# Kernel optimization log

Hardware: AMD Instinct MI355X
Metric: run time of the kernel (lower is better)

Reference implementation:

```python
import jax, jax.numpy as jnp
import numpy as np

NUM_FEATURES = 128   # conv spatial length
WINDOW = 128         # conv channels / lstm seq len
KC = 16              # kernels per group
KS = 3               # conv kernel size
FC1 = 32             # number of independent LSTMs
H = 32               # lstm hidden size
NL = 2               # lstm layers
PAD = 1
POOL_LEN = (NUM_FEATURES + 2 * PAD) // 2  # maxpool(k=2,s=2,p=1) output length
B = 128


def setup_inputs():
    key = jax.random.key(0)
    ks = jax.random.split(key, 13)
    x = jax.random.normal(ks[0], (B, WINDOW, NUM_FEATURES), jnp.float32)
    conv_w = jax.random.normal(ks[1], (WINDOW * KC, 1, KS), jnp.float32) * 0.3
    conv_b = jax.random.normal(ks[2], (WINDOW * KC,), jnp.float32) * 0.1
    fc1_in = KC * POOL_LEN
    fc1_w = jax.random.normal(ks[3], (FC1, fc1_in), jnp.float32) * 0.02
    fc1_b = jax.random.normal(ks[4], (FC1,), jnp.float32) * 0.02
    w_ih0 = jax.random.normal(ks[5], (FC1, 4 * H), jnp.float32) * 0.1          # layer0, input size 1
    w_ih1 = jax.random.normal(ks[6], (NL - 1, FC1, 4 * H, H), jnp.float32) * 0.1
    w_hh = jax.random.normal(ks[7], (NL, FC1, 4 * H, H), jnp.float32) * 0.1
    b_lstm = jax.random.normal(ks[8], (NL, FC1, 4 * H), jnp.float32) * 0.1     # bias_ih + bias_hh combined
    mu_w = jax.random.normal(ks[9], (1, FC1 * H), jnp.float32) * 0.05
    mu_b = jax.random.normal(ks[10], (1,), jnp.float32) * 0.05
    lv_w = jax.random.normal(ks[11], (1, FC1 * H), jnp.float32) * 0.05
    lv_b = jax.random.normal(ks[12], (1,), jnp.float32) * 0.05
    return {"x": x, "conv_w": conv_w, "conv_b": conv_b, "fc1_w": fc1_w, "fc1_b": fc1_b,
            "w_ih0": w_ih0, "w_ih1": w_ih1, "w_hh": w_hh, "b_lstm": b_lstm,
            "mu_w": mu_w, "mu_b": mu_b, "lv_w": lv_w, "lv_b": lv_b}


def _lstm_cell(gates, c_prev):
    # torch gate order: i, f, g, o
    i, f, g, o = jnp.split(gates, 4, axis=-1)
    c_new = jax.nn.sigmoid(f) * c_prev + jax.nn.sigmoid(i) * jnp.tanh(g)
    h_new = jax.nn.sigmoid(o) * jnp.tanh(c_new)
    return h_new, c_new


def reference(x, conv_w, conv_b, fc1_w, fc1_b, w_ih0, w_ih1, w_hh, b_lstm, mu_w, mu_b, lv_w, lv_b):
    bsz = x.shape[0]
    # grouped conv1d: groups = WINDOW, each group maps 1 -> KC channels
    y = jax.lax.conv_general_dilated(x, conv_w, window_strides=(1,), padding=[(PAD, PAD)],
                                     feature_group_count=WINDOW,
                                     dimension_numbers=('NCH', 'OIH', 'NCH'))
    y = jax.nn.relu(y + conv_b[None, :, None])
    neg = jnp.finfo(y.dtype).min
    y = jnp.pad(y, ((0, 0), (0, 0), (PAD, PAD)), constant_values=neg)
    y = y.reshape(bsz, WINDOW * KC, POOL_LEN, 2).max(axis=-1)
    # regroup to [B, WINDOW, KC*POOL_LEN] (channel layout = group-major, matches torch view)
    y = y.reshape(bsz, WINDOW, KC * POOL_LEN)
    z = jnp.einsum('bwi,oi->bwo', y, fc1_w) + fc1_b   # [B, WINDOW, FC1]

    # FC1 independent NL-layer LSTMs batched over the feature axis; time axis = WINDOW
    h0 = jnp.zeros((NL, bsz, FC1, H), z.dtype)
    c0 = jnp.zeros_like(h0)

    def step(carry, x_t):  # x_t: [B, FC1]
        h, c = carry
        hs, cs = [], []
        gates = jnp.einsum('bf,fg->bfg', x_t, w_ih0) + jnp.einsum('bfh,fgh->bfg', h[0], w_hh[0]) + b_lstm[0]
        h_l, c_l = _lstm_cell(gates, c[0])
        hs.append(h_l); cs.append(c_l)
        for l in range(1, NL):
            gates = (jnp.einsum('bfh,fgh->bfg', h_l, w_ih1[l - 1])
                     + jnp.einsum('bfh,fgh->bfg', h[l], w_hh[l]) + b_lstm[l])
            h_l, c_l = _lstm_cell(gates, c[l])
            hs.append(h_l); cs.append(c_l)
        return (jnp.stack(hs), jnp.stack(cs)), None

    (h_fin, _), _ = jax.lax.scan(step, (h0, c0), jnp.transpose(z, (1, 0, 2)))
    combined = h_fin[-1].reshape(bsz, FC1 * H)  # top layer, last step; feature-major like torch.cat
    mu = combined @ mu_w.T + mu_b
    log_var = combined @ lv_w.T + lv_b
    sigma = jnp.exp(0.5 * log_var)
    return (mu - 1.96 * sigma, mu, mu + 1.96 * sigma, log_var)
```

## Files before the change

kernel.cpp:

```cpp
#include <hip/hip_runtime.h>
#include <hip/hip_bf16.h>
#include <math.h>

#define BATCH 128
#define WIN   128
#define NF    128
#define KC    16
#define POOL  65
#define NFC1  32
#define HS    32
#define LW    40
#define KP    1056
#define PSTR  1064

typedef float f32x4 __attribute__((ext_vector_type(4)));
typedef short bf16x8 __attribute__((ext_vector_type(8)));

#define LOG2E   1.442695041f
#define LOG2E2  2.885390082f

__device__ __forceinline__ float cellf(float& c, float gi, float gf, float gg, float go) {
    float ei = __builtin_amdgcn_exp2f(gi);
    float ef = __builtin_amdgcn_exp2f(gf);
    float eg = __builtin_amdgcn_exp2f(gg);
    float eo = __builtin_amdgcn_exp2f(go);
    float sf = __builtin_amdgcn_rcpf(1.f + ef);
    c = fmaf(sf, c, (eg - 1.f) * __builtin_amdgcn_rcpf((1.f + ei) * (eg + 1.f)));
    float ec = __builtin_amdgcn_exp2f(__builtin_amdgcn_fmed3f(c, -30.f, 30.f) * LOG2E2);
    return (ec - 1.f) * __builtin_amdgcn_rcpf((1.f + eo) * (ec + 1.f));
}
__device__ __forceinline__ unsigned short f2bf(float x) {
    __hip_bfloat16 h = __float2bfloat16(x);
    unsigned short u; __builtin_memcpy(&u, &h, 2); return u;
}
__device__ __forceinline__ float bf2f(unsigned short u) {
    unsigned int v = ((unsigned int)u) << 16;
    float f; __builtin_memcpy(&f, &v, 4); return f;
}
__device__ __forceinline__ bf16x8 load_row8_scaled(const float* row, float sc) {
    float4 lo = ((const float4*)row)[0];
    float4 hi = ((const float4*)row)[1];
    union { bf16x8 v; unsigned short u[8]; } t;
    t.u[0] = f2bf(lo.x * sc); t.u[1] = f2bf(lo.y * sc); t.u[2] = f2bf(lo.z * sc); t.u[3] = f2bf(lo.w * sc);
    t.u[4] = f2bf(hi.x * sc); t.u[5] = f2bf(hi.y * sc); t.u[6] = f2bf(hi.z * sc); t.u[7] = f2bf(hi.w * sc);
    return t.v;
}

__global__ __launch_bounds__(256) void k0_wconv(
    const float* __restrict__ fc1_w, unsigned short* __restrict__ w_bf)
{
    const int o = blockIdx.x;
    for (int i = threadIdx.x; i < KP; i += 256) {
        float v = (i < KC * POOL) ? fc1_w[(size_t)o * (KC * POOL) + i] : 0.f;
        w_bf[(size_t)o * KP + i] = f2bf(v);
    }
}

__global__ __launch_bounds__(256, 4) void k1_conv_fc1(
    const float* __restrict__ x, const float* __restrict__ conv_w, const float* __restrict__ conv_b,
    const unsigned short* __restrict__ w_bf, const float* __restrict__ fc1_b, float* __restrict__ z)
{
    __shared__ __align__(16) unsigned short xp[16][132];
    __shared__ __align__(16) unsigned short poolb[16 * PSTR];
    __shared__ float cw[KC][3];
    __shared__ float cb[KC];
    __shared__ float fb[NFC1];

    const int w = blockIdx.x >> 3;
    const int bbase = (blockIdx.x & 7) * 16;
    const int tid = threadIdx.x;

    if (tid < KC * 3) cw[tid / 3][tid % 3] = conv_w[(w * KC + tid / 3) * 3 + tid % 3];
    if (tid >= 64 && tid < 64 + KC) cb[tid - 64] = conv_b[w * KC + (tid - 64)];
    if (tid >= 96 && tid < 96 + NFC1) fb[tid - 96] = fc1_b[tid - 96];

    for (int i = tid; i < 16 * 32; i += 256) {
        int b = i >> 5, q = i & 31;
        float4 v = ((const float4*)(x + (size_t)(bbase + b) * (WIN * NF) + (size_t)w * NF))[q];
        unsigned short* dst = &xp[b][1 + q * 4];
        dst[0] = f2bf(v.x); dst[1] = f2bf(v.y); dst[2] = f2bf(v.z); dst[3] = f2bf(v.w);
    }
    if (tid < 16) { xp[tid][0] = 0; xp[tid][129] = 0; xp[tid][130] = 0; xp[tid][131] = 0; }
    __syncthreads();

    {
        const int b = tid >> 4;
        const int k = tid & 15;
        const float w0 = cw[k][0], w1 = cw[k][1], w2 = cw[k][2], bb = cb[k];
        float v1 = 0.f;
        float v2 = bf2f(xp[b][0]);
        float v3 = bf2f(xp[b][1]);
        unsigned short* prow = &poolb[b * PSTR + k * POOL];
        #pragma unroll 5
        for (int j = 0; j < POOL; ++j) {
            float v0 = v1; v1 = v2; v2 = v3;
            v3 = bf2f(xp[b][2 * j + 2]);
            float oa = bb + w0 * v0 + w1 * v1 + w2 * v2;
            float ob = bb + w0 * v1 + w1 * v2 + w2 * v3;
            float m = 0.f;
            if (j > 0)        m = fmaxf(m, oa);
            if (j < POOL - 1) m = fmaxf(m, ob);
            prow[j] = f2bf(m);
        }
    }
    for (int i = tid; i < 16 * (KP - KC * POOL); i += 256) {
        int b = i >> 4, c = i & 15;
        poolb[b * PSTR + KC * POOL + c] = 0;
    }
    __syncthreads();

    const int lane = tid & 63;
    const int wid = tid >> 6;
    if (wid < 2) {
        const int col = lane & 15;
        const int kg = lane >> 4;
        const int g = wid * 16 + col;
        f32x4 acc;
        {
            float bias = fb[g];
            acc[0] = bias; acc[1] = bias; acc[2] = bias; acc[3] = bias;
        }
        const unsigned short* wrow = w_bf + (size_t)g * KP;
        #pragma unroll 4
        for (int ks = 0; ks < KP / 32; ++ks) {
            bf16x8 aP = *(const bf16x8*)&poolb[col * PSTR + ks * 32 + kg * 8];
            bf16x8 bW = *(const bf16x8*)&wrow[ks * 32 + kg * 8];
            acc = __builtin_amdgcn_mfma_f32_16x16x32_bf16(aP, bW, acc, 0, 0, 0);
        }
        float4 st; st.x = acc[0]; st.y = acc[1]; st.z = acc[2]; st.w = acc[3];
        *(float4*)&z[(size_t)w * (NFC1 * BATCH) + (size_t)g * BATCH + bbase + kg * 4] = st;
    }
}

__global__ __launch_bounds__(256, 1) void k2_lstm_mfma(
    const float* __restrict__ w_ih0, const float* __restrict__ w_ih1,
    const float* __restrict__ w_hh, const float* __restrict__ b_lstm,
    const float* __restrict__ z, float* __restrict__ h1fin)
{
    __shared__ float zs[WIN][16];
    __shared__ __align__(16) unsigned short h0b0[16 * LW];
    __shared__ __align__(16) unsigned short h0b1[16 * LW];
    __shared__ __align__(16) unsigned short h1b0[16 * LW];
    __shared__ __align__(16) unsigned short h1b1[16 * LW];

    const int f = blockIdx.x >> 3;
    const int bbase = (blockIdx.x & 7) * 16;
    const int tid = threadIdx.x;
    const int wid = tid >> 6, lane = tid & 63;
    const bool isL0 = (wid < 2);
    const int s = wid & 1;
    const int col = lane & 15;
    const int kg = lane >> 4;

    for (int i = tid; i < WIN * 4; i += 256) {
        int t = i >> 2, q = i & 3;
        ((float4*)&zs[t][0])[q] = ((const float4*)&z[(size_t)t * (NFC1 * BATCH) + f * BATCH + bbase])[q];
    }
    for (int i = tid; i < 16 * LW; i += 256) {
        h0b0[i] = 0; h0b1[i] = 0; h1b0[i] = 0; h1b1[i] = 0;
    }

    const float gsc[4] = { -LOG2E, -LOG2E, LOG2E2, -LOG2E };

    const float* WA = isL0 ? (w_hh + (size_t)f * 4096)
                           : (w_ih1 + (size_t)f * 4096);
    const float* WV = w_hh + (size_t)(NFC1 + f) * 4096;
    bf16x8 fA[4], fB[4];
    float bias[4], wi0[4];
    const int loff = isL0 ? 0 : (NFC1 * 128);
    #pragma unroll
    for (int gi = 0; gi < 4; ++gi) {
        int nt = gi * 2 + s;
        int g = nt * 16 + col;
        fA[gi] = load_row8_scaled(WA + g * 32 + kg * 8, gsc[gi]);
        if (!isL0) fB[gi] = load_row8_scaled(WV + g * 32 + kg * 8, gsc[gi]);
        bias[gi] = b_lstm[loff + f * 128 + g] * gsc[gi];
        wi0[gi] = w_ih0[f * 128 + g] * gsc[gi];
    }
    __syncthreads();

    const int hread = col * LW + kg * 8;
    const int hw0 = (kg * 4 + 0) * LW + 16 * s + col;
    float cst[4] = {0.f, 0.f, 0.f, 0.f};
    f32x4 zv = *(const f32x4*)&zs[0][kg * 4];

    auto body = [&](int it, const unsigned short* h0r, unsigned short* h0w,
                            const unsigned short* h1r, unsigned short* h1w) {
        if (isL0) {
            if (it < WIN) {
                bf16x8 hA = *(const bf16x8*)&h0r[hread];
                f32x4 aI, aF, aG, aO;
                #pragma unroll
                for (int j = 0; j < 4; ++j) {
                    aI[j] = fmaf(zv[j], wi0[0], bias[0]);
                    aF[j] = fmaf(zv[j], wi0[1], bias[1]);
                    aG[j] = fmaf(zv[j], wi0[2], bias[2]);
                    aO[j] = fmaf(zv[j], wi0[3], bias[3]);
                }
                aI = __builtin_amdgcn_mfma_f32_16x16x32_bf16(hA, fA[0], aI, 0, 0, 0);
                aF = __builtin_amdgcn_mfma_f32_16x16x32_bf16(hA, fA[1], aF, 0, 0, 0);
                aG = __builtin_amdgcn_mfma_f32_16x16x32_bf16(hA, fA[2], aG, 0, 0, 0);
                aO = __builtin_amdgcn_mfma_f32_16x16x32_bf16(hA, fA[3], aO, 0, 0, 0);
                if (it + 1 < WIN) zv = *(const f32x4*)&zs[it + 1][kg * 4];
                #pragma unroll
                for (int j = 0; j < 4; ++j) {
                    float h = cellf(cst[j], aI[j], aF[j], aG[j], aO[j]);
                    h0w[hw0 + j * LW] = f2bf(h);
                }
            }
        } else {
            if (it >= 1) {
                bf16x8 hA = *(const bf16x8*)&h0r[hread];
                bf16x8 hB = *(const bf16x8*)&h1r[hread];
                f32x4 aI, aF, aG, aO;
                #pragma unroll
                for (int j = 0; j < 4; ++j) { aI[j] = bias[0]; aF[j] = bias[1]; aG[j] = bias[2]; aO[j] = bias[3]; }
                aI = __builtin_amdgcn_mfma_f32_16x16x32_bf16(hA, fA[0], aI, 0, 0, 0);
                aI = __builtin_amdgcn_mfma_f32_16x16x32_bf16(hB, fB[0], aI, 0, 0, 0);
                aF = __builtin_amdgcn_mfma_f32_16x16x32_bf16(hA, fA[1], aF, 0, 0, 0);
                aF = __builtin_amdgcn_mfma_f32_16x16x32_bf16(hB, fB[1], aF, 0, 0, 0);
                aG = __builtin_amdgcn_mfma_f32_16x16x32_bf16(hA, fA[2], aG, 0, 0, 0);
                aG = __builtin_amdgcn_mfma_f32_16x16x32_bf16(hB, fB[2], aG, 0, 0, 0);
                aO = __builtin_amdgcn_mfma_f32_16x16x32_bf16(hA, fA[3], aO, 0, 0, 0);
                aO = __builtin_amdgcn_mfma_f32_16x16x32_bf16(hB, fB[3], aO, 0, 0, 0);
                if (it < WIN) {
                    #pragma unroll
                    for (int j = 0; j < 4; ++j) {
                        float h = cellf(cst[j], aI[j], aF[j], aG[j], aO[j]);
                        h1w[hw0 + j * LW] = f2bf(h);
                    }
                } else {
                    #pragma unroll
                    for (int j = 0; j < 4; ++j) {
                        float h = cellf(cst[j], aI[j], aF[j], aG[j], aO[j]);
                        h1fin[(size_t)(bbase + kg * 4 + j) * (NFC1 * HS) + f * HS + 16 * s + col] = h;
                    }
                }
            }
        }
    };

    body(0, h0b0, h0b1, h1b0, h1b1);
    __syncthreads();
    #pragma unroll 1
    for (int it = 1; it <= WIN; it += 2) {
        body(it,     h0b1, h0b0, h1b1, h1b0);
        __syncthreads();
        body(it + 1, h0b0, h0b1, h1b0, h1b1);
        __syncthreads();
    }
}

__global__ __launch_bounds__(128) void k3_head(
    const float* __restrict__ h1fin, const float* __restrict__ mu_w, const float* __restrict__ mu_b,
    const float* __restrict__ lv_w, const float* __restrict__ lv_b, float* __restrict__ out)
{
    const int b = blockIdx.x, tid = threadIdx.x;
    const float* hrow = h1fin + (size_t)b * (NFC1 * HS);
    float am = 0.f, al = 0.f;
    for (int i = tid; i < NFC1 * HS; i += 128) {
        float h = hrow[i];
        am = fmaf(h, mu_w[i], am);
        al = fmaf(h, lv_w[i], al);
    }
    for (int off = 32; off >= 1; off >>= 1) {
        am += __shfl_down(am, off, 64);
        al += __shfl_down(al, off, 64);
    }
    __shared__ float sm[2], sl[2];
    const int wv = tid >> 6, ln = tid & 63;
    if (ln == 0) { sm[wv] = am; sl[wv] = al; }
    __syncthreads();
    if (tid == 0) {
        float mu = sm[0] + sm[1] + mu_b[0];
        float lv = sl[0] + sl[1] + lv_b[0];
        float sg = expf(0.5f * lv);
        out[b]           = mu - 1.96f * sg;
        out[128 + b]     = mu;
        out[256 + b]     = mu + 1.96f * sg;
        out[384 + b]     = lv;
    }
}

extern "C" void kernel_launch(void* const* d_in, const int* in_sizes, int n_in,
                              void* d_out, int out_size, void* d_ws, size_t ws_size,
                              hipStream_t stream)
{
    const float* x      = (const float*)d_in[0];
    const float* conv_w = (const float*)d_in[1];
    const float* conv_b = (const float*)d_in[2];
    const float* fc1_w  = (const float*)d_in[3];
    const float* fc1_b  = (const float*)d_in[4];
    const float* w_ih0  = (const float*)d_in[5];
    const float* w_ih1  = (const float*)d_in[6];
    const float* w_hh   = (const float*)d_in[7];
    const float* b_lstm = (const float*)d_in[8];
    const float* mu_w   = (const float*)d_in[9];
    const float* mu_b   = (const float*)d_in[10];
    const float* lv_w   = (const float*)d_in[11];
    const float* lv_b   = (const float*)d_in[12];
    float* out = (float*)d_out;

    float* z     = (float*)d_ws;
    float* h1fin = z + (size_t)WIN * NFC1 * BATCH;
    unsigned short* w_bf = (unsigned short*)(h1fin + (size_t)BATCH * NFC1 * HS);

    k0_wconv<<<dim3(NFC1), dim3(256), 0, stream>>>(fc1_w, w_bf);
    k1_conv_fc1<<<dim3(WIN * 8), dim3(256), 0, stream>>>(x, conv_w, conv_b, w_bf, fc1_b, z);
    k2_lstm_mfma<<<dim3(NFC1 * 8), dim3(256), 0, stream>>>(w_ih0, w_ih1, w_hh, b_lstm, z, h1fin);
    k3_head<<<dim3(BATCH), dim3(128), 0, stream>>>(h1fin, mu_w, mu_b, lv_w, lv_b, out);
}
```

Before: 83.47 us.

## Replace block barriers in LSTM kernel with per-wave LDS flag handshakes

The LSTM recurrence kernel now synchronises its layer-0 and layer-1 waves through LDS flag counters with spin-waits instead of a __syncthreads per timestep. Layer-0 h state gets a 4-deep ring buffer so layer 0 can run up to a few steps ahead of layer 1, and each wave waits only on the producers it actually depends on. The aim is to cut barrier overhead and let the two layers pipeline more loosely. It risks spin-wait cost, correctness issues with LDS memory ordering, and the loss of the simple lockstep structure.

```diff
diff --git a/kernel.cpp b/kernel.cpp
--- a/kernel.cpp
+++ b/kernel.cpp
@@ -44,6 +44,9 @@
     t.u[0] = f2bf(lo.x * sc); t.u[1] = f2bf(lo.y * sc); t.u[2] = f2bf(lo.z * sc); t.u[3] = f2bf(lo.w * sc);
     t.u[4] = f2bf(hi.x * sc); t.u[5] = f2bf(hi.y * sc); t.u[6] = f2bf(hi.z * sc); t.u[7] = f2bf(hi.w * sc);
     return t.v;
+}
+__device__ __forceinline__ void waitge(const int* f, int t) {
+    while (*(const volatile int*)f < t) { }
 }
 
 __global__ __launch_bounds__(256) void k0_wconv(
@@ -138,10 +141,9 @@
     const float* __restrict__ z, float* __restrict__ h1fin)
 {
     __shared__ float zs[WIN][16];
-    __shared__ __align__(16) unsigned short h0b0[16 * LW];
-    __shared__ __align__(16) unsigned short h0b1[16 * LW];
-    __shared__ __align__(16) unsigned short h1b0[16 * LW];
-    __shared__ __align__(16) unsigned short h1b1[16 * LW];
+    __shared__ __align__(16) unsigned short h0r_[4][16 * LW];
+    __shared__ __align__(16) unsigned short h1r_[2][16 * LW];
+    __shared__ int flg[4];
 
     const int f = blockIdx.x >> 3;
     const int bbase = (blockIdx.x & 7) * 16;
@@ -157,11 +159,12 @@
         ((float4*)&zs[t][0])[q] = ((const float4*)&z[(size_t)t * (NFC1 * BATCH) + f * BATCH + bbase])[q];
     }
     for (int i = tid; i < 16 * LW; i += 256) {
-        h0b0[i] = 0; h0b1[i] = 0; h1b0[i] = 0; h1b1[i] = 0;
-    }
+        h0r_[0][i] = 0; h0r_[1][i] = 0; h0r_[2][i] = 0; h0r_[3][i] = 0;
+        h1r_[0][i] = 0; h1r_[1][i] = 0;
+    }
+    if (tid < 4) flg[tid] = -1;
 
     const float gsc[4] = { -LOG2E, -LOG2E, LOG2E2, -LOG2E };
-
     const float* WA = isL0 ? (w_hh + (size_t)f * 4096)
                            : (w_ih1 + (size_t)f * 4096);
     const float* WV = w_hh + (size_t)(NFC1 + f) * 4096;
@@ -182,72 +185,75 @@
     const int hread = col * LW + kg * 8;
     const int hw0 = (kg * 4 + 0) * LW + 16 * s + col;
     float cst[4] = {0.f, 0.f, 0.f, 0.f};
-    f32x4 zv = *(const f32x4*)&zs[0][kg * 4];
-
-    auto body = [&](int it, const unsigned short* h0r, unsigned short* h0w,
-                            const unsigned short* h1r, unsigned short* h1w) {
-        if (isL0) {
-            if (it < WIN) {
-                bf16x8 hA = *(const bf16x8*)&h0r[hread];
-                f32x4 aI, aF, aG, aO;
-                #pragma unroll
-                for (int j = 0; j < 4; ++j) {
-                    aI[j] = fmaf(zv[j], wi0[0], bias[0]);
-                    aF[j] = fmaf(zv[j], wi0[1], bias[1]);
-                    aG[j] = fmaf(zv[j], wi0[2], bias[2]);
-                    aO[j] = fmaf(zv[j], wi0[3], bias[3]);
-                }
-                aI = __builtin_amdgcn_mfma_f32_16x16x32_bf16(hA, fA[0], aI, 0, 0, 0);
-                aF = __builtin_amdgcn_mfma_f32_16x16x32_bf16(hA, fA[1], aF, 0, 0, 0);
-                aG = __builtin_amdgcn_mfma_f32_16x16x32_bf16(hA, fA[2], aG, 0, 0, 0);
-                aO = __builtin_amdgcn_mfma_f32_16x16x32_bf16(hA, fA[3], aO, 0, 0, 0);
-                if (it + 1 < WIN) zv = *(const f32x4*)&zs[it + 1][kg * 4];
+
+    if (isL0) {
+        f32x4 zv = *(const f32x4*)&zs[0][kg * 4];
+        #pragma unroll 1
+        for (int t = 0; t < WIN; ++t) {
+            waitge(&flg[1 - s], t - 1);
+            waitge(&flg[2], t - 4);
+            waitge(&flg[3], t - 4);
+            __builtin_amdgcn_sched_barrier(0);
+            bf16x8 hA = *(const bf16x8*)&h0r_[(t + 3) & 3][hread];
+            f32x4 aI, aF, aG, aO;
+            #pragma unroll
+            for (int j = 0; j < 4; ++j) {
+                aI[j] = fmaf(zv[j], wi0[0], bias[0]);
+                aF[j] = fmaf(zv[j], wi0[1], bias[1]);
+                aG[j] = fmaf(zv[j], wi0[2], bias[2]);
+                aO[j] = fmaf(zv[j], wi0[3], bias[3]);
+            }
+            aI = __builtin_amdgcn_mfma_f32_16x16x32_bf16(hA, fA[0], aI, 0, 0, 0);
+            aF = __builtin_amdgcn_mfma_f32_16x16x32_bf16(hA, fA[1], aF, 0, 0, 0);
+            aG = __builtin_amdgcn_mfma_f32_16x16x32_bf16(hA, fA[2], aG, 0, 0, 0);
+            aO = __builtin_amdgcn_mfma_f32_16x16x32_bf16(hA, fA[3], aO, 0, 0, 0);
+            if (t + 1 < WIN) zv = *(const f32x4*)&zs[t + 1][kg * 4];
+            unsigned short* wbuf = &h0r_[t & 3][0];
+            #pragma unroll
+            for (int j = 0; j < 4; ++j) {
+                float h = cellf(cst[j], aI[j], aF[j], aG[j], aO[j]);
+                wbuf[hw0 + j * LW] = f2bf(h);
+            }
+            asm volatile("s_waitcnt lgkmcnt(0)" ::: "memory");
+            if (lane == 0) *(volatile int*)&flg[s] = t;
+        }
+    } else {
+        #pragma unroll 1
+        for (int t = 0; t < WIN; ++t) {
+            waitge(&flg[0], t);
+            waitge(&flg[1], t);
+            waitge(&flg[3 - s], t - 1);
+            __builtin_amdgcn_sched_barrier(0);
+            bf16x8 hA = *(const bf16x8*)&h0r_[t & 3][hread];
+            bf16x8 hB = *(const bf16x8*)&h1r_[(t + 1) & 1][hread];
+            f32x4 aI, aF, aG, aO;
+            #pragma unroll
+            for (int j = 0; j < 4; ++j) { aI[j] = bias[0]; aF[j] = bias[1]; aG[j] = bias[2]; aO[j] = bias[3]; }
+            aI = __builtin_amdgcn_mfma_f32_16x16x32_bf16(hA, fA[0], aI, 0, 0, 0);
+            aI = __builtin_amdgcn_mfma_f32_16x16x32_bf16(hB, fB[0], aI, 0, 0, 0);
+            aF = __builtin_amdgcn_mfma_f32_16x16x32_bf16(hA, fA[1], aF, 0, 0, 0);
+            aF = __builtin_amdgcn_mfma_f32_16x16x32_bf16(hB, fB[1], aF, 0, 0, 0);
+            aG = __builtin_amdgcn_mfma_f32_16x16x32_bf16(hA, fA[2], aG, 0, 0, 0);
+            aG = __builtin_amdgcn_mfma_f32_16x16x32_bf16(hB, fB[2], aG, 0, 0, 0);
+            aO = __builtin_amdgcn_mfma_f32_16x16x32_bf16(hA, fA[3], aO, 0, 0, 0);
+            aO = __builtin_amdgcn_mfma_f32_16x16x32_bf16(hB, fB[3], aO, 0, 0, 0);
+            if (t < WIN - 1) {
+                unsigned short* wbuf = &h1r_[t & 1][0];
                 #pragma unroll
                 for (int j = 0; j < 4; ++j) {
                     float h = cellf(cst[j], aI[j], aF[j], aG[j], aO[j]);
-                    h0w[hw0 + j * LW] = f2bf(h);
+                    wbuf[hw0 + j * LW] = f2bf(h);
+                }
+                asm volatile("s_waitcnt lgkmcnt(0)" ::: "memory");
+                if (lane == 0) *(volatile int*)&flg[2 + s] = t;
+            } else {
+                #pragma unroll
+                for (int j = 0; j < 4; ++j) {
+                    float h = cellf(cst[j], aI[j], aF[j], aG[j], aO[j]);
+                    h1fin[(size_t)(bbase + kg * 4 + j) * (NFC1 * HS) + f * HS + 16 * s + col] = h;
                 }
             }
-        } else {
-            if (it >= 1) {
-                bf16x8 hA = *(const bf16x8*)&h0r[hread];
-                bf16x8 hB = *(const bf16x8*)&h1r[hread];
-                f32x4 aI, aF, aG, aO;
-                #pragma unroll
-                for (int j = 0; j < 4; ++j) { aI[j] = bias[0]; aF[j] = bias[1]; aG[j] = bias[2]; aO[j] = bias[3]; }
-                aI = __builtin_amdgcn_mfma_f32_16x16x32_bf16(hA, fA[0], aI, 0, 0, 0);
-                aI = __builtin_amdgcn_mfma_f32_16x16x32_bf16(hB, fB[0], aI, 0, 0, 0);
-                aF = __builtin_amdgcn_mfma_f32_16x16x32_bf16(hA, fA[1], aF, 0, 0, 0);
-                aF = __builtin_amdgcn_mfma_f32_16x16x32_bf16(hB, fB[1], aF, 0, 0, 0);
-                aG = __builtin_amdgcn_mfma_f32_16x16x32_bf16(hA, fA[2], aG, 0, 0, 0);
-                aG = __builtin_amdgcn_mfma_f32_16x16x32_bf16(hB, fB[2], aG, 0, 0, 0);
-                aO = __builtin_amdgcn_mfma_f32_16x16x32_bf16(hA, fA[3], aO, 0, 0, 0);
-                aO = __builtin_amdgcn_mfma_f32_16x16x32_bf16(hB, fB[3], aO, 0, 0, 0);
-                if (it < WIN) {
-                    #pragma unroll
-                    for (int j = 0; j < 4; ++j) {
-                        float h = cellf(cst[j], aI[j], aF[j], aG[j], aO[j]);
-                        h1w[hw0 + j * LW] = f2bf(h);
-                    }
-                } else {
-                    #pragma unroll
-                    for (int j = 0; j < 4; ++j) {
-                        float h = cellf(cst[j], aI[j], aF[j], aG[j], aO[j]);
-                        h1fin[(size_t)(bbase + kg * 4 + j) * (NFC1 * HS) + f * HS + 16 * s + col] = h;
-                    }
-                }
-            }
-        }
-    };
-
-    body(0, h0b0, h0b1, h1b0, h1b1);
-    __syncthreads();
-    #pragma unroll 1
-    for (int it = 1; it <= WIN; it += 2) {
-        body(it,     h0b1, h0b0, h1b1, h1b0);
-        __syncthreads();
-        body(it + 1, h0b0, h0b1, h1b0, h1b1);
-        __syncthreads();
+        }
     }
 }
 
```

New measurement: 106.3 us. 27.4% more time.
